# Kernel tuning notes

Hardware: AMD Instinct MI355X
Metric: run time of the kernel (lower is better)

Reference implementation:

```python
import jax, jax.numpy as jnp
import numpy as np

N_HEADS = 4
NEG_SLOPE = 0.2  # DGL GATConv default leaky_relu slope


def setup_inputs() -> dict:
    key = jax.random.key(0)
    ks = jax.random.split(key, 12)
    N, E = 50000, 800000
    in_dim, time_dim, out_dim = 128, 128, 128
    d_head = out_dim // N_HEADS
    in_total = in_dim + time_dim
    h = jax.random.normal(ks[0], (N, in_dim), jnp.float32)
    time_tensor = jax.random.uniform(ks[1], (E,), jnp.float32)
    src = jax.random.randint(ks[2], (E,), 0, N, jnp.int32)
    dst = jax.random.randint(ks[3], (E,), 0, N, jnp.int32)
    # TimeEncoding: Linear(1, time_dim) with xavier weight, zero bias
    w_t = jax.random.normal(ks[4], (time_dim, 1), jnp.float32) * (6.0 / (1 + time_dim)) ** 0.5
    b_t = jnp.zeros((time_dim,), jnp.float32)
    # GATConv params
    W_fc = jax.random.normal(ks[5], (N_HEADS * d_head, in_total), jnp.float32) * (2.0 / in_total) ** 0.5
    attn_l = jax.random.normal(ks[6], (N_HEADS, d_head), jnp.float32) * 0.1
    attn_r = jax.random.normal(ks[7], (N_HEADS, d_head), jnp.float32) * 0.1
    W_res = jax.random.normal(ks[8], (N_HEADS * d_head, in_total), jnp.float32) * (2.0 / in_total) ** 0.5
    bias = jnp.zeros((N_HEADS * d_head,), jnp.float32)
    return {"h": h, "time_tensor": time_tensor, "src": src, "dst": dst,
            "num_nodes": N, "w_t": w_t, "b_t": b_t, "W_fc": W_fc,
            "attn_l": attn_l, "attn_r": attn_r, "W_res": W_res, "bias": bias}


def reference(h, time_tensor, src, dst, num_nodes, w_t, b_t, W_fc, attn_l, attn_r, W_res, bias):
    N = num_nodes
    E = src.shape[0]
    # Time encoding: cos(W t + b), per edge -> [E, time_dim]
    time_emb = jnp.cos(time_tensor[:, None] * w_t[:, 0][None, :] + b_t[None, :])
    # Mailbox mean of concat([src h, time_emb]) per dst node.
    # mean(concat) == concat(mean, mean), so sum the two halves separately.
    ones = jnp.ones((E,), h.dtype)
    deg = jax.ops.segment_sum(ones, dst, num_segments=N)  # [N]
    sum_h = jax.ops.segment_sum(h[src], dst, num_segments=N)       # [N, in_dim]
    sum_t = jax.ops.segment_sum(time_emb, dst, num_segments=N)     # [N, time_dim]
    inv_deg = 1.0 / jnp.maximum(deg, 1.0)
    h_time = jnp.concatenate([sum_h, sum_t], axis=1) * inv_deg[:, None]  # [N, in+time]
    # GATConv (eval mode, no dropout)
    d_head = W_fc.shape[0] // N_HEADS
    feat = (h_time @ W_fc.T).reshape(N, N_HEADS, d_head)  # [N,H,D]
    el = jnp.sum(feat * attn_l[None], axis=-1)  # [N,H]
    er = jnp.sum(feat * attn_r[None], axis=-1)  # [N,H]
    e = el[src] + er[dst]                        # [E,H]
    e = jnp.where(e > 0, e, NEG_SLOPE * e)
    # edge softmax over incoming edges of each dst node
    m = jax.ops.segment_max(e, dst, num_segments=N)  # [N,H]
    m = jnp.where(jnp.isfinite(m), m, 0.0)
    ex = jnp.exp(e - m[dst])
    denom = jax.ops.segment_sum(ex, dst, num_segments=N)
    a = ex / jnp.maximum(denom[dst], 1e-9)           # [E,H]
    rst = jax.ops.segment_sum(a[:, :, None] * feat[src], dst, num_segments=N)  # [N,H,D]
    res = (h_time @ W_res.T).reshape(N, N_HEADS, d_head)
    out = rst + res + bias.reshape(1, N_HEADS, d_head)
    out = jax.nn.elu(out)
    return out.reshape(N, -1)  # [N, out_dim]
```

## Files before the change

kernel.cpp:

```cpp
#include <hip/hip_runtime.h>
#include <math.h>

#define NH 4
#define NEG_SLOPE 0.2f
#define BKT_SHIFT 8
#define EPB 4096
#define CBLK 8192
#define TBLK 2048
#define INV2PI 0.15915494309189535f
#define LOG2E  1.4426950408889634f

typedef __attribute__((ext_vector_type(8))) short bf16x8;
typedef __attribute__((ext_vector_type(4))) float f32x4;
typedef __attribute__((ext_vector_type(2))) float f32x2;

__device__ __forceinline__ float blo(unsigned u) { return __uint_as_float(u << 16); }
__device__ __forceinline__ float bhi(unsigned u) { return __uint_as_float(u & 0xFFFF0000u); }
__device__ __forceinline__ f32x2 mk2(float a, float b) { f32x2 r; r.x = a; r.y = b; return r; }
__device__ __forceinline__ f32x2 unpk(unsigned u) { return mk2(blo(u), bhi(u)); }
__device__ __forceinline__ unsigned short rne(float f) {
    unsigned u = __float_as_uint(f);
    u += 0x7FFFu + ((u >> 16) & 1u);
    return (unsigned short)(u >> 16);
}
__device__ __forceinline__ unsigned pack2(float a, float b) {
    return (unsigned)rne(a) | ((unsigned)rne(b) << 16);
}

__global__ __launch_bounds__(256) void k_prep(
    const float* __restrict__ h, unsigned* __restrict__ hbu, int n_pairs,
    const float* __restrict__ Wfc, const float* __restrict__ Wres,
    unsigned* __restrict__ wcat,
    const float* __restrict__ w_t, const float* __restrict__ b_t,
    float* __restrict__ tbl,
    const int* __restrict__ dst, int* __restrict__ bkt_cnt, int E, int NB, int EB) {
    __shared__ int cnt[256];
    int tid = threadIdx.x;
    int t = blockIdx.x * blockDim.x + tid;
    if (t < n_pairs) {
        float2 v = ((const float2*)h)[t];
        hbu[t] = pack2(v.x, v.y);
    }
    if (t < 32768) {
        int col = t >> 7, kk = t & 127;
        const float* srcp = (col < 128) ? (Wfc + (size_t)col * 256)
                                        : (Wres + (size_t)(col - 128) * 256);
        float2 v = ((const float2*)srcp)[kk];
        int s  = col >> 6, ct = (col >> 4) & 3, r = col & 15;
        int ks = kk >> 4,  q  = (kk >> 2) & 3,  d = kk & 3;
        int w2i = ((s * 32 + ks * 4 + ct) << 8) + ((q * 16 + r) << 2) + d;
        wcat[w2i] = pack2(v.x, v.y);
    }
    if (blockIdx.x < (unsigned)EB) {
        cnt[tid] = 0;
        __syncthreads();
        int q0 = (blockIdx.x * CBLK) >> 2;
#pragma unroll
        for (int k = 0; k < CBLK / 1024; k++) {
            int qi = q0 + k * 256 + tid;
            int base = qi * 4;
            if (base + 3 < E) {
                int4 dd = ((const int4*)dst)[qi];
                atomicAdd(&cnt[dd.x >> BKT_SHIFT], 1);
                atomicAdd(&cnt[dd.y >> BKT_SHIFT], 1);
                atomicAdd(&cnt[dd.z >> BKT_SHIFT], 1);
                atomicAdd(&cnt[dd.w >> BKT_SHIFT], 1);
            } else {
                for (int e = base; e < E; e++) atomicAdd(&cnt[dst[e] >> BKT_SHIFT], 1);
            }
        }
        __syncthreads();
        if (tid < NB) {
            int c = cnt[tid];
            if (c) atomicAdd(bkt_cnt + tid, c);
        }
    }
    int tb = blockIdx.x - EB;
    if (tb >= 0 && tb < TBLK) {
        int idx = tb * 256 + tid;
        int j = idx >> 7, d = idx & 127;
        float wv = w_t[d] * INV2PI;
        float bv = b_t[d] * INV2PI;
        float tv = ((float)j + 0.5f) * (1.0f / 4096.0f);
        tbl[idx] = __builtin_amdgcn_cosf(fmaf(tv, wv, bv));
    }
}

__global__ __launch_bounds__(256) void k_bktscan(
    const int* __restrict__ bkt_cnt, int* __restrict__ bkt_start,
    int* __restrict__ bkt_cursor, int* __restrict__ row_start,
    int NB, int E, int N) {
    __shared__ int wsum[4];
    int tid = threadIdx.x, lane = tid & 63, wid = tid >> 6;
    int v = (tid < NB) ? bkt_cnt[tid] : 0;
    int x = v;
#pragma unroll
    for (int off = 1; off < 64; off <<= 1) {
        int y = __shfl_up(x, off, 64);
        if (lane >= off) x += y;
    }
    if (lane == 63) wsum[wid] = x;
    __syncthreads();
    if (tid == 0) {
        int s = 0;
#pragma unroll
        for (int k = 0; k < 4; k++) { int tk = wsum[k]; wsum[k] = s; s += tk; }
    }
    __syncthreads();
    int excl = wsum[wid] + x - v;
    if (tid < NB) { bkt_start[tid] = excl; bkt_cursor[tid] = excl; }
    if (tid == 0) { bkt_start[NB] = E; row_start[N] = E; }
}

__global__ __launch_bounds__(256) void k_binscatter(
    const int* __restrict__ src, const int* __restrict__ dst,
    const float* __restrict__ tt, int* __restrict__ bkt_cursor,
    uint2* __restrict__ staged, int E, int NB) {
    __shared__ int cnt[1024];
    __shared__ int basep[1024];
    int e0 = blockIdx.x * EPB;
    int tid = threadIdx.x;
    for (int b = tid; b < NB; b += 256) cnt[b] = 0;
    __syncthreads();
#pragma unroll
    for (int k = 0; k < EPB / 256; k++) {
        int e = e0 + k * 256 + tid;
        if (e < E) atomicAdd(&cnt[dst[e] >> BKT_SHIFT], 1);
    }
    __syncthreads();
    for (int b = tid; b < NB; b += 256) {
        int c = cnt[b];
        basep[b] = (c > 0) ? atomicAdd(bkt_cursor + b, c) : 0;
        cnt[b] = 0;
    }
    __syncthreads();
#pragma unroll
    for (int k = 0; k < EPB / 256; k++) {
        int e = e0 + k * 256 + tid;
        if (e < E) {
            int d = dst[e];
            int b = d >> BKT_SHIFT;
            int r = atomicAdd(&cnt[b], 1);
            unsigned tq = min((unsigned)(tt[e] * 32768.0f), 32767u);
            staged[basep[b] + r] =
                make_uint2(((unsigned)src[e] << 15) | tq, (unsigned)(d & 255));
        }
    }
}

__global__ __launch_bounds__(256) void k_binsort(
    const uint2* __restrict__ staged, const int* __restrict__ bkt_start,
    int* __restrict__ row_start, unsigned* __restrict__ est, int N) {
    __shared__ int cnt[256];
    __shared__ int cur[256];
    __shared__ int wsum[4];
    int b = blockIdx.x;
    int n0 = b << BKT_SHIFT;
    int tid = threadIdx.x;
    cnt[tid] = 0;
    __syncthreads();
    int s0 = bkt_start[b], s1 = bkt_start[b + 1];
    for (int p = s0 + tid; p < s1; p += 256)
        atomicAdd(&cnt[staged[p].y], 1);
    __syncthreads();
    int lane = tid & 63, wid = tid >> 6;
    int v = cnt[tid];
    int x = v;
#pragma unroll
    for (int off = 1; off < 64; off <<= 1) {
        int y = __shfl_up(x, off, 64);
        if (lane >= off) x += y;
    }
    if (lane == 63) wsum[wid] = x;
    __syncthreads();
    if (tid == 0) {
        int s = 0;
#pragma unroll
        for (int k = 0; k < 4; k++) { int tk = wsum[k]; wsum[k] = s; s += tk; }
    }
    __syncthreads();
    int excl = s0 + wsum[wid] + x - v;
    cur[tid] = excl;
    if (n0 + tid < N) row_start[n0 + tid] = excl;
    __syncthreads();
    for (int p = s0 + tid; p < s1; p += 256) {
        uint2 vv = staged[p];
        int pos = atomicAdd(&cur[vv.y], 1);
        est[pos] = vv.x;
    }
}

__device__ __forceinline__ void agg_edge(unsigned u, const char* __restrict__ hb,
                                         const char* __restrict__ tb, int i,
                                         f32x2* aH, f32x2* aT) {
    unsigned hoff = (u >> 15) << 8;
    unsigned toff = (u & 0x7FF8u) << 6;
    uint4 hv = *(const uint4*)(hb + hoff + i * 16);
    const f32x4* cp = (const f32x4*)(tb + toff + i * 32);
    f32x4 c0 = cp[0], c1 = cp[1];
    aH[0] += unpk(hv.x);
    aH[1] += unpk(hv.y);
    aH[2] += unpk(hv.z);
    aH[3] += unpk(hv.w);
    aT[0] += mk2(c0.x, c0.y);
    aT[1] += mk2(c0.z, c0.w);
    aT[2] += mk2(c1.x, c1.y);
    aT[3] += mk2(c1.z, c1.w);
}

__device__ __forceinline__ void attn_edge(unsigned u, const char* __restrict__ fb,
                                          int i, int hd, const char* __restrict__ elb,
                                          float erh, f32x2* acc, float& den) {
    unsigned off = (u >> 15) << 8;
    float elh = *(const float*)(elb + (off >> 4) + (hd << 2));
    uint4 fv = *(const uint4*)(fb + off + i * 16);
    float w = elh + erh; w = w > 0.f ? w : NEG_SLOPE * w;
    float ex = __builtin_amdgcn_exp2f(w);
    f32x2 ex2 = mk2(ex, ex);
    acc[0] = ex2 * unpk(fv.x) + acc[0];
    acc[1] = ex2 * unpk(fv.y) + acc[1];
    acc[2] = ex2 * unpk(fv.z) + acc[2];
    acc[3] = ex2 * unpk(fv.w) + acc[3];
    den += ex;
}

__global__ __launch_bounds__(256) void k_agg(
    const unsigned* __restrict__ hbu, const float* __restrict__ tbl,
    const unsigned* __restrict__ est, const int* __restrict__ row_start,
    unsigned* __restrict__ htu, int N) {
    int lane = threadIdx.x & 63;
    int g = lane >> 4, i = lane & 15;
    int wid = blockIdx.x * 4 + (threadIdx.x >> 6);
    int nw = gridDim.x * 4;
    const char* hb = (const char*)hbu;
    const char* tb = (const char*)tbl;
    for (int n = wid; n < N; n += nw) {
        int rs = row_start[n], re = row_start[n + 1];
        f32x2 aH[4] = {}, aT[4] = {};
        int nb = (re - rs) >> 4;
        int e = rs + g;
        for (int j = 0; j < nb; j++, e += 16) {
            unsigned u0 = est[e];
            unsigned u1 = est[e + 4];
            unsigned u2 = est[e + 8];
            unsigned u3 = est[e + 12];
            agg_edge(u0, hb, tb, i, aH, aT);
            agg_edge(u1, hb, tb, i, aH, aT);
            agg_edge(u2, hb, tb, i, aH, aT);
            agg_edge(u3, hb, tb, i, aH, aT);
        }
        for (; e < re; e += 4)
            agg_edge(est[e], hb, tb, i, aH, aT);
#pragma unroll
        for (int off = 16; off <= 32; off <<= 1) {
#pragma unroll
            for (int k = 0; k < 4; k++) {
                aH[k].x += __shfl_xor(aH[k].x, off, 64);
                aH[k].y += __shfl_xor(aH[k].y, off, 64);
                aT[k].x += __shfl_xor(aT[k].x, off, 64);
                aT[k].y += __shfl_xor(aT[k].y, off, 64);
            }
        }
        if (g == 0) {
            int deg = re - rs;
            float idg = (deg > 0) ? 1.0f / (float)deg : 1.0f;
            uint4* ht4 = (uint4*)htu;
            uint4 oh, ot;
            oh.x = pack2(aH[0].x * idg, aH[0].y * idg);
            oh.y = pack2(aH[1].x * idg, aH[1].y * idg);
            oh.z = pack2(aH[2].x * idg, aH[2].y * idg);
            oh.w = pack2(aH[3].x * idg, aH[3].y * idg);
            ot.x = pack2(aT[0].x * idg, aT[0].y * idg);
            ot.y = pack2(aT[1].x * idg, aT[1].y * idg);
            ot.z = pack2(aT[2].x * idg, aT[2].y * idg);
            ot.w = pack2(aT[3].x * idg, aT[3].y * idg);
            ht4[(size_t)n * 32 + i]      = oh;
            ht4[(size_t)n * 32 + 16 + i] = ot;
        }
    }
}

__global__ __launch_bounds__(256) void k_gemm(
    const unsigned short* __restrict__ ht, const unsigned* __restrict__ wcat,
    unsigned short* __restrict__ feat, float* __restrict__ res_out, int N) {
    __shared__ __align__(16) unsigned short As[64 * 264];
    int tid = threadIdx.x;
    int row0 = blockIdx.x * 64;
    const uint4* src4 = (const uint4*)ht;
    for (int idx = tid; idx < 64 * 32; idx += 256) {
        int rl = idx >> 5, c16 = idx & 31;
        int gr = row0 + rl; if (gr >= N) gr = N - 1;
        uint4 v = src4[(size_t)gr * 32 + c16];
        *(uint4*)(As + rl * 264 + c16 * 8) = v;
    }
    __syncthreads();
    int wave = tid >> 6, lane = tid & 63;
    int r = lane & 15, q = lane >> 4;
    int colbase = wave * 64;
    const bf16x8* bbase = (const bf16x8*)wcat + (size_t)wave * 2048 + lane;
    const unsigned short* abase = As + r * 264 + q * 8;
    f32x4 acc[4][4] = {};
#pragma unroll
    for (int ks = 0; ks < 8; ks++) {
        bf16x8 a[4], b[4];
#pragma unroll
        for (int rt = 0; rt < 4; rt++)
            a[rt] = *(const bf16x8*)(abase + rt * (16 * 264) + ks * 32);
#pragma unroll
        for (int ct = 0; ct < 4; ct++)
            b[ct] = bbase[(ks * 4 + ct) * 64];
#pragma unroll
        for (int rt = 0; rt < 4; rt++)
#pragma unroll
            for (int ct = 0; ct < 4; ct++)
                acc[rt][ct] = __builtin_amdgcn_mfma_f32_16x16x32_bf16(a[rt], b[ct], acc[rt][ct], 0, 0, 0);
    }
    bool featw = (colbase < 128);
#pragma unroll
    for (int rt = 0; rt < 4; rt++) {
        int rb = row0 + rt * 16 + q * 4;
#pragma unroll
        for (int ct = 0; ct < 4; ct++) {
            int col = colbase + ct * 16 + r;
#pragma unroll
            for (int reg = 0; reg < 4; reg++) {
                int row = rb + reg;
                if (row >= N) continue;
                float v = acc[rt][ct][reg];
                if (featw) feat[(size_t)row * 128 + col] = rne(v);
                else       res_out[(size_t)row * 128 + (col - 128)] = v;
            }
        }
    }
}

__global__ void k_el_er(const unsigned* __restrict__ featu,
                        const float* __restrict__ attn_l, const float* __restrict__ attn_r,
                        float* __restrict__ el, float* __restrict__ er, int NH4) {
    int t = blockIdx.x * blockDim.x + threadIdx.x;
    if (t >= NH4) return;
    int n = t >> 2, hd = t & 3;
    const unsigned* f = featu + (size_t)n * 64 + hd * 16;
    const float2* al = (const float2*)(attn_l + hd * 32);
    const float2* ar = (const float2*)(attn_r + hd * 32);
    float sl = 0.f, sr = 0.f;
#pragma unroll
    for (int i = 0; i < 16; i++) {
        unsigned u = f[i];
        float f0 = blo(u), f1 = bhi(u);
        float2 a = al[i], b = ar[i];
        sl = fmaf(f0, a.x, fmaf(f1, a.y, sl));
        sr = fmaf(f0, b.x, fmaf(f1, b.y, sr));
    }
    el[t] = sl * LOG2E;
    er[t] = sr * LOG2E;
}

__global__ __launch_bounds__(256) void k_attn(
    const unsigned* __restrict__ est, const int* __restrict__ row_start,
    const float* __restrict__ el, const float* __restrict__ er,
    const unsigned* __restrict__ featu, const float* __restrict__ bias,
    float* __restrict__ out, int N) {
    int lane = threadIdx.x & 63;
    int g = lane >> 4, i = lane & 15;
    int hd = i >> 2;
    int wid = blockIdx.x * 4 + (threadIdx.x >> 6);
    int nw = gridDim.x * 4;
    const char* fb = (const char*)featu;
    const char* elb = (const char*)el;
    for (int n = wid; n < N; n += nw) {
        int rs = row_start[n], re = row_start[n + 1];
        float erh = er[(size_t)n * 4 + hd];
        f32x2 acc[4] = {};
        float den = 0.f;
        int nb = (re - rs) >> 4;
        int e = rs + g;
        for (int j = 0; j < nb; j++, e += 16) {
            unsigned u0 = est[e];
            unsigned u1 = est[e + 4];
            unsigned u2 = est[e + 8];
            unsigned u3 = est[e + 12];
            attn_edge(u0, fb, i, hd, elb, erh, acc, den);
            attn_edge(u1, fb, i, hd, elb, erh, acc, den);
            attn_edge(u2, fb, i, hd, elb, erh, acc, den);
            attn_edge(u3, fb, i, hd, elb, erh, acc, den);
        }
        for (; e < re; e += 4)
            attn_edge(est[e], fb, i, hd, elb, erh, acc, den);
#pragma unroll
        for (int off = 16; off <= 32; off <<= 1) {
#pragma unroll
            for (int k = 0; k < 4; k++) {
                acc[k].x += __shfl_xor(acc[k].x, off, 64);
                acc[k].y += __shfl_xor(acc[k].y, off, 64);
            }
            den += __shfl_xor(den, off, 64);
        }
        if (g == 0) {
            float id = 1.0f / fmaxf(den, 1e-9f);
            float* op = out + (size_t)n * 128 + i * 8;
            const float* bp = bias + i * 8;
            float4 o0 = ((const float4*)op)[0], o1 = ((const float4*)op)[1];
            float4 b0 = ((const float4*)bp)[0], b1 = ((const float4*)bp)[1];
            float4 r0, r1;
            r0.x = fmaf(acc[0].x, id, o0.x + b0.x);
            r0.y = fmaf(acc[0].y, id, o0.y + b0.y);
            r0.z = fmaf(acc[1].x, id, o0.z + b0.z);
            r0.w = fmaf(acc[1].y, id, o0.w + b0.w);
            r1.x = fmaf(acc[2].x, id, o1.x + b1.x);
            r1.y = fmaf(acc[2].y, id, o1.y + b1.y);
            r1.z = fmaf(acc[3].x, id, o1.z + b1.z);
            r1.w = fmaf(acc[3].y, id, o1.w + b1.w);
            r0.x = r0.x > 0.f ? r0.x : (__expf(r0.x) - 1.0f);
            r0.y = r0.y > 0.f ? r0.y : (__expf(r0.y) - 1.0f);
            r0.z = r0.z > 0.f ? r0.z : (__expf(r0.z) - 1.0f);
            r0.w = r0.w > 0.f ? r0.w : (__expf(r0.w) - 1.0f);
            r1.x = r1.x > 0.f ? r1.x : (__expf(r1.x) - 1.0f);
            r1.y = r1.y > 0.f ? r1.y : (__expf(r1.y) - 1.0f);
            r1.z = r1.z > 0.f ? r1.z : (__expf(r1.z) - 1.0f);
            r1.w = r1.w > 0.f ? r1.w : (__expf(r1.w) - 1.0f);
            ((float4*)op)[0] = r0;
            ((float4*)op)[1] = r1;
        }
    }
}

extern "C" void kernel_launch(void* const* d_in, const int* in_sizes, int n_in,
                              void* d_out, int out_size, void* d_ws, size_t ws_size,
                              hipStream_t stream) {
    const float* h     = (const float*)d_in[0];
    const float* tt    = (const float*)d_in[1];
    const int*   src   = (const int*)d_in[2];
    const int*   dst   = (const int*)d_in[3];
    const float* w_t   = (const float*)d_in[5];
    const float* b_t   = (const float*)d_in[6];
    const float* W_fc  = (const float*)d_in[7];
    const float* al    = (const float*)d_in[8];
    const float* ar    = (const float*)d_in[9];
    const float* W_res = (const float*)d_in[10];
    const float* bias  = (const float*)d_in[11];

    int N = in_sizes[0] / 128;
    int E = in_sizes[1];
    int NB = (N + 255) >> BKT_SHIFT;
    int EB = (E + CBLK - 1) / CBLK;

    char* ws = (char*)d_ws;
    size_t off = 0;
    auto alloc = [&](size_t bytes) { void* p = ws + off; off = (off + bytes + 15) & ~(size_t)15; return p; };
    unsigned* htu     = (unsigned*)alloc((size_t)N * 128 * 4);
    unsigned* hbu     = (unsigned*)alloc((size_t)N * 64 * 4);
    unsigned* featu   = (unsigned*)alloc((size_t)N * 64 * 4);
    unsigned* wcat    = (unsigned*)alloc(32768 * 4);
    float*    tbl     = (float*)alloc((size_t)4096 * 128 * 4);
    float*    el      = (float*)alloc((size_t)N * NH * 4);
    float*    er      = (float*)alloc((size_t)N * NH * 4);
    int*      row_st  = (int*)alloc((size_t)(N + 1) * 4);
    int*      bkt_cur = (int*)alloc((size_t)NB * 4);
    int*      bkt_cnt = (int*)alloc((size_t)NB * 4);
    int*      bkt_sta = (int*)alloc((size_t)(NB + 1) * 4);
    unsigned* est     = (unsigned*)alloc((size_t)E * 4);
    uint2*    staged  = (uint2*)featu;

    hipMemsetAsync(bkt_cnt, 0, (size_t)NB * 4, stream);

    int prep_n = N * 64;
    hipLaunchKernelGGL(k_prep, dim3((prep_n + 255) / 256), dim3(256), 0, stream,
                       h, hbu, prep_n, W_fc, W_res, wcat, w_t, b_t, tbl,
                       dst, bkt_cnt, E, NB, EB);
    hipLaunchKernelGGL(k_bktscan, dim3(1), dim3(256), 0, stream,
                       bkt_cnt, bkt_sta, bkt_cur, row_st, NB, E, N);
    hipLaunchKernelGGL(k_binscatter, dim3((E + EPB - 1) / EPB), dim3(256), 0, stream,
                       src, dst, tt, bkt_cur, staged, E, NB);
    hipLaunchKernelGGL(k_binsort, dim3(NB), dim3(256), 0, stream,
                       staged, bkt_sta, row_st, est, N);
    int npersist = min((N + 3) / 4, 2048);
    hipLaunchKernelGGL(k_agg, dim3(npersist), dim3(256), 0, stream,
                       hbu, tbl, est, row_st, htu, N);
    hipLaunchKernelGGL(k_gemm, dim3((N + 63) / 64), dim3(256), 0, stream,
                       (const unsigned short*)htu, wcat,
                       (unsigned short*)featu, (float*)d_out, N);
    hipLaunchKernelGGL(k_el_er, dim3((N * NH + 255) / 256), dim3(256), 0, stream,
                       featu, al, ar, el, er, N * NH);
    hipLaunchKernelGGL(k_attn, dim3(npersist), dim3(256), 0, stream,
                       est, row_st, el, er, featu, bias, (float*)d_out, N);
}
```

Measured before the change: 275.3 us.

## Assign one 16-lane group per node in aggregation and attention kernels

Replaces the persistent one-wave-per-node scheme in k_agg and k_attn with a non-persistent grid where each 16-thread group handles a whole destination node. All edges of a node are walked serially in chunks of four, with a padded masked tail, so the cross-group shuffle reduction disappears. This removes lanes left idle for low-degree nodes (average degree is about 16) and the reduction cost. In exchange, each lane has a longer serial dependency chain, and high-degree nodes can cause load imbalance within a wave.

Result: faster. 257.4 us (-6.5%).

```diff
diff --git a/kernel.cpp b/kernel.cpp
--- a/kernel.cpp
+++ b/kernel.cpp
@@ -190,7 +190,7 @@
     }
 }
 
-__device__ __forceinline__ void agg_edge(unsigned u, const char* __restrict__ hb,
+__device__ __forceinline__ void agg_edge(unsigned u, float wgt, const char* __restrict__ hb,
                                          const char* __restrict__ tb, int i,
                                          f32x2* aH, f32x2* aT) {
     unsigned hoff = (u >> 15) << 8;
@@ -198,24 +198,25 @@
     uint4 hv = *(const uint4*)(hb + hoff + i * 16);
     const f32x4* cp = (const f32x4*)(tb + toff + i * 32);
     f32x4 c0 = cp[0], c1 = cp[1];
-    aH[0] += unpk(hv.x);
-    aH[1] += unpk(hv.y);
-    aH[2] += unpk(hv.z);
-    aH[3] += unpk(hv.w);
-    aT[0] += mk2(c0.x, c0.y);
-    aT[1] += mk2(c0.z, c0.w);
-    aT[2] += mk2(c1.x, c1.y);
-    aT[3] += mk2(c1.z, c1.w);
-}
-
-__device__ __forceinline__ void attn_edge(unsigned u, const char* __restrict__ fb,
+    f32x2 w2 = mk2(wgt, wgt);
+    aH[0] = w2 * unpk(hv.x) + aH[0];
+    aH[1] = w2 * unpk(hv.y) + aH[1];
+    aH[2] = w2 * unpk(hv.z) + aH[2];
+    aH[3] = w2 * unpk(hv.w) + aH[3];
+    aT[0] = w2 * mk2(c0.x, c0.y) + aT[0];
+    aT[1] = w2 * mk2(c0.z, c0.w) + aT[1];
+    aT[2] = w2 * mk2(c1.x, c1.y) + aT[2];
+    aT[3] = w2 * mk2(c1.z, c1.w) + aT[3];
+}
+
+__device__ __forceinline__ void attn_edge(unsigned u, bool valid, const char* __restrict__ fb,
                                           int i, int hd, const char* __restrict__ elb,
                                           float erh, f32x2* acc, float& den) {
     unsigned off = (u >> 15) << 8;
     float elh = *(const float*)(elb + (off >> 4) + (hd << 2));
     uint4 fv = *(const uint4*)(fb + off + i * 16);
     float w = elh + erh; w = w > 0.f ? w : NEG_SLOPE * w;
-    float ex = __builtin_amdgcn_exp2f(w);
+    float ex = valid ? __builtin_amdgcn_exp2f(w) : 0.f;
     f32x2 ex2 = mk2(ex, ex);
     acc[0] = ex2 * unpk(fv.x) + acc[0];
     acc[1] = ex2 * unpk(fv.y) + acc[1];
@@ -228,56 +229,49 @@
     const unsigned* __restrict__ hbu, const float* __restrict__ tbl,
     const unsigned* __restrict__ est, const int* __restrict__ row_start,
     unsigned* __restrict__ htu, int N) {
-    int lane = threadIdx.x & 63;
-    int g = lane >> 4, i = lane & 15;
-    int wid = blockIdx.x * 4 + (threadIdx.x >> 6);
-    int nw = gridDim.x * 4;
+    int tid = threadIdx.x;
+    int i = tid & 15;
+    int n = blockIdx.x * 16 + (tid >> 4);
+    if (n >= N) return;
     const char* hb = (const char*)hbu;
     const char* tb = (const char*)tbl;
-    for (int n = wid; n < N; n += nw) {
-        int rs = row_start[n], re = row_start[n + 1];
-        f32x2 aH[4] = {}, aT[4] = {};
-        int nb = (re - rs) >> 4;
-        int e = rs + g;
-        for (int j = 0; j < nb; j++, e += 16) {
-            unsigned u0 = est[e];
-            unsigned u1 = est[e + 4];
-            unsigned u2 = est[e + 8];
-            unsigned u3 = est[e + 12];
-            agg_edge(u0, hb, tb, i, aH, aT);
-            agg_edge(u1, hb, tb, i, aH, aT);
-            agg_edge(u2, hb, tb, i, aH, aT);
-            agg_edge(u3, hb, tb, i, aH, aT);
-        }
-        for (; e < re; e += 4)
-            agg_edge(est[e], hb, tb, i, aH, aT);
-#pragma unroll
-        for (int off = 16; off <= 32; off <<= 1) {
-#pragma unroll
-            for (int k = 0; k < 4; k++) {
-                aH[k].x += __shfl_xor(aH[k].x, off, 64);
-                aH[k].y += __shfl_xor(aH[k].y, off, 64);
-                aT[k].x += __shfl_xor(aT[k].x, off, 64);
-                aT[k].y += __shfl_xor(aT[k].y, off, 64);
-            }
-        }
-        if (g == 0) {
-            int deg = re - rs;
-            float idg = (deg > 0) ? 1.0f / (float)deg : 1.0f;
-            uint4* ht4 = (uint4*)htu;
-            uint4 oh, ot;
-            oh.x = pack2(aH[0].x * idg, aH[0].y * idg);
-            oh.y = pack2(aH[1].x * idg, aH[1].y * idg);
-            oh.z = pack2(aH[2].x * idg, aH[2].y * idg);
-            oh.w = pack2(aH[3].x * idg, aH[3].y * idg);
-            ot.x = pack2(aT[0].x * idg, aT[0].y * idg);
-            ot.y = pack2(aT[1].x * idg, aT[1].y * idg);
-            ot.z = pack2(aT[2].x * idg, aT[2].y * idg);
-            ot.w = pack2(aT[3].x * idg, aT[3].y * idg);
-            ht4[(size_t)n * 32 + i]      = oh;
-            ht4[(size_t)n * 32 + 16 + i] = ot;
-        }
-    }
+    int rs = row_start[n], re = row_start[n + 1];
+    f32x2 aH[4] = {}, aT[4] = {};
+    int e = rs;
+    int nfull = (re - rs) >> 2;
+    for (int j = 0; j < nfull; j++, e += 4) {
+        unsigned u0 = est[e];
+        unsigned u1 = est[e + 1];
+        unsigned u2 = est[e + 2];
+        unsigned u3 = est[e + 3];
+        agg_edge(u0, 1.0f, hb, tb, i, aH, aT);
+        agg_edge(u1, 1.0f, hb, tb, i, aH, aT);
+        agg_edge(u2, 1.0f, hb, tb, i, aH, aT);
+        agg_edge(u3, 1.0f, hb, tb, i, aH, aT);
+    }
+    if (e < re) {
+        unsigned u0 = est[e];
+        bool v1 = e + 1 < re, v2 = e + 2 < re;
+        unsigned u1 = v1 ? est[e + 1] : u0;
+        unsigned u2 = v2 ? est[e + 2] : u0;
+        agg_edge(u0, 1.0f, hb, tb, i, aH, aT);
+        agg_edge(u1, v1 ? 1.0f : 0.0f, hb, tb, i, aH, aT);
+        agg_edge(u2, v2 ? 1.0f : 0.0f, hb, tb, i, aH, aT);
+    }
+    int deg = re - rs;
+    float idg = (deg > 0) ? 1.0f / (float)deg : 1.0f;
+    uint4* ht4 = (uint4*)htu;
+    uint4 oh, ot;
+    oh.x = pack2(aH[0].x * idg, aH[0].y * idg);
+    oh.y = pack2(aH[1].x * idg, aH[1].y * idg);
+    oh.z = pack2(aH[2].x * idg, aH[2].y * idg);
+    oh.w = pack2(aH[3].x * idg, aH[3].y * idg);
+    ot.x = pack2(aT[0].x * idg, aT[0].y * idg);
+    ot.y = pack2(aT[1].x * idg, aT[1].y * idg);
+    ot.z = pack2(aT[2].x * idg, aT[2].y * idg);
+    ot.w = pack2(aT[3].x * idg, aT[3].y * idg);
+    ht4[(size_t)n * 32 + i]      = oh;
+    ht4[(size_t)n * 32 + 16 + i] = ot;
 }
 
 __global__ __launch_bounds__(256) void k_gemm(
@@ -361,68 +355,62 @@
     const float* __restrict__ el, const float* __restrict__ er,
     const unsigned* __restrict__ featu, const float* __restrict__ bias,
     float* __restrict__ out, int N) {
-    int lane = threadIdx.x & 63;
-    int g = lane >> 4, i = lane & 15;
+    int tid = threadIdx.x;
+    int i = tid & 15;
     int hd = i >> 2;
-    int wid = blockIdx.x * 4 + (threadIdx.x >> 6);
-    int nw = gridDim.x * 4;
+    int n = blockIdx.x * 16 + (tid >> 4);
+    if (n >= N) return;
+    int rs = row_start[n], re = row_start[n + 1];
+    float erh = er[(size_t)n * 4 + hd];
     const char* fb = (const char*)featu;
     const char* elb = (const char*)el;
-    for (int n = wid; n < N; n += nw) {
-        int rs = row_start[n], re = row_start[n + 1];
-        float erh = er[(size_t)n * 4 + hd];
-        f32x2 acc[4] = {};
-        float den = 0.f;
-        int nb = (re - rs) >> 4;
-        int e = rs + g;
-        for (int j = 0; j < nb; j++, e += 16) {
-            unsigned u0 = est[e];
-            unsigned u1 = est[e + 4];
-            unsigned u2 = est[e + 8];
-            unsigned u3 = est[e + 12];
-            attn_edge(u0, fb, i, hd, elb, erh, acc, den);
-            attn_edge(u1, fb, i, hd, elb, erh, acc, den);
-            attn_edge(u2, fb, i, hd, elb, erh, acc, den);
-            attn_edge(u3, fb, i, hd, elb, erh, acc, den);
-        }
-        for (; e < re; e += 4)
-            attn_edge(est[e], fb, i, hd, elb, erh, acc, den);
-#pragma unroll
-        for (int off = 16; off <= 32; off <<= 1) {
-#pragma unroll
-            for (int k = 0; k < 4; k++) {
-                acc[k].x += __shfl_xor(acc[k].x, off, 64);
-                acc[k].y += __shfl_xor(acc[k].y, off, 64);
-            }
-            den += __shfl_xor(den, off, 64);
-        }
-        if (g == 0) {
-            float id = 1.0f / fmaxf(den, 1e-9f);
-            float* op = out + (size_t)n * 128 + i * 8;
-            const float* bp = bias + i * 8;
-            float4 o0 = ((const float4*)op)[0], o1 = ((const float4*)op)[1];
-            float4 b0 = ((const float4*)bp)[0], b1 = ((const float4*)bp)[1];
-            float4 r0, r1;
-            r0.x = fmaf(acc[0].x, id, o0.x + b0.x);
-            r0.y = fmaf(acc[0].y, id, o0.y + b0.y);
-            r0.z = fmaf(acc[1].x, id, o0.z + b0.z);
-            r0.w = fmaf(acc[1].y, id, o0.w + b0.w);
-            r1.x = fmaf(acc[2].x, id, o1.x + b1.x);
-            r1.y = fmaf(acc[2].y, id, o1.y + b1.y);
-            r1.z = fmaf(acc[3].x, id, o1.z + b1.z);
-            r1.w = fmaf(acc[3].y, id, o1.w + b1.w);
-            r0.x = r0.x > 0.f ? r0.x : (__expf(r0.x) - 1.0f);
-            r0.y = r0.y > 0.f ? r0.y : (__expf(r0.y) - 1.0f);
-            r0.z = r0.z > 0.f ? r0.z : (__expf(r0.z) - 1.0f);
-            r0.w = r0.w > 0.f ? r0.w : (__expf(r0.w) - 1.0f);
-            r1.x = r1.x > 0.f ? r1.x : (__expf(r1.x) - 1.0f);
-            r1.y = r1.y > 0.f ? r1.y : (__expf(r1.y) - 1.0f);
-            r1.z = r1.z > 0.f ? r1.z : (__expf(r1.z) - 1.0f);
-            r1.w = r1.w > 0.f ? r1.w : (__expf(r1.w) - 1.0f);
-            ((float4*)op)[0] = r0;
-            ((float4*)op)[1] = r1;
-        }
-    }
+    f32x2 acc[4] = {};
+    float den = 0.f;
+    int e = rs;
+    int nfull = (re - rs) >> 2;
+    for (int j = 0; j < nfull; j++, e += 4) {
+        unsigned u0 = est[e];
+        unsigned u1 = est[e + 1];
+        unsigned u2 = est[e + 2];
+        unsigned u3 = est[e + 3];
+        attn_edge(u0, true, fb, i, hd, elb, erh, acc, den);
+        attn_edge(u1, true, fb, i, hd, elb, erh, acc, den);
+        attn_edge(u2, true, fb, i, hd, elb, erh, acc, den);
+        attn_edge(u3, true, fb, i, hd, elb, erh, acc, den);
+    }
+    if (e < re) {
+        unsigned u0 = est[e];
+        bool v1 = e + 1 < re, v2 = e + 2 < re;
+        unsigned u1 = v1 ? est[e + 1] : u0;
+        unsigned u2 = v2 ? est[e + 2] : u0;
+        attn_edge(u0, true, fb, i, hd, elb, erh, acc, den);
+        attn_edge(u1, v1, fb, i, hd, elb, erh, acc, den);
+        attn_edge(u2, v2, fb, i, hd, elb, erh, acc, den);
+    }
+    float id = 1.0f / fmaxf(den, 1e-9f);
+    float* op = out + (size_t)n * 128 + i * 8;
+    const float* bp = bias + i * 8;
+    float4 o0 = ((const float4*)op)[0], o1 = ((const float4*)op)[1];
+    float4 b0 = ((const float4*)bp)[0], b1 = ((const float4*)bp)[1];
+    float4 r0, r1;
+    r0.x = fmaf(acc[0].x, id, o0.x + b0.x);
+    r0.y = fmaf(acc[0].y, id, o0.y + b0.y);
+    r0.z = fmaf(acc[1].x, id, o0.z + b0.z);
+    r0.w = fmaf(acc[1].y, id, o0.w + b0.w);
+    r1.x = fmaf(acc[2].x, id, o1.x + b1.x);
+    r1.y = fmaf(acc[2].y, id, o1.y + b1.y);
+    r1.z = fmaf(acc[3].x, id, o1.z + b1.z);
+    r1.w = fmaf(acc[3].y, id, o1.w + b1.w);
+    r0.x = r0.x > 0.f ? r0.x : (__expf(r0.x) - 1.0f);
+    r0.y = r0.y > 0.f ? r0.y : (__expf(r0.y) - 1.0f);
+    r0.z = r0.z > 0.f ? r0.z : (__expf(r0.z) - 1.0f);
+    r0.w = r0.w > 0.f ? r0.w : (__expf(r0.w) - 1.0f);
+    r1.x = r1.x > 0.f ? r1.x : (__expf(r1.x) - 1.0f);
+    r1.y = r1.y > 0.f ? r1.y : (__expf(r1.y) - 1.0f);
+    r1.z = r1.z > 0.f ? r1.z : (__expf(r1.z) - 1.0f);
+    r1.w = r1.w > 0.f ? r1.w : (__expf(r1.w) - 1.0f);
+    ((float4*)op)[0] = r0;
+    ((float4*)op)[1] = r1;
 }
 
 extern "C" void kernel_launch(void* const* d_in, const int* in_sizes, int n_in,
@@ -474,14 +462,13 @@
                        src, dst, tt, bkt_cur, staged, E, NB);
     hipLaunchKernelGGL(k_binsort, dim3(NB), dim3(256), 0, stream,
                        staged, bkt_sta, row_st, est, N);
-    int npersist = min((N + 3) / 4, 2048);
-    hipLaunchKernelGGL(k_agg, dim3(npersist), dim3(256), 0, stream,
+    hipLaunchKernelGGL(k_agg, dim3((N + 15) / 16), dim3(256), 0, stream,
                        hbu, tbl, est, row_st, htu, N);
     hipLaunchKernelGGL(k_gemm, dim3((N + 63) / 64), dim3(256), 0, stream,
                        (const unsigned short*)htu, wcat,
                        (unsigned short*)featu, (float*)d_out, N);
     hipLaunchKernelGGL(k_el_er, dim3((N * NH + 255) / 256), dim3(256), 0, stream,
                        featu, al, ar, el, er, N * NH);
-    hipLaunchKernelGGL(k_attn, dim3(npersist), dim3(256), 0, stream,
+    hipLaunchKernelGGL(k_attn, dim3((N + 15) / 16), dim3(256), 0, stream,
                        est, row_st, el, er, featu, bias, (float*)d_out, N);
 }
```
